# Kernel tuning notes

Measured on AMD Instinct MI355X. Metric: run time of the kernel, lower is better.

## Reference

```python
import jax, jax.numpy as jnp
import numpy as np
from jax import lax

EPS = 1e-5

def conv3x3(x, w, b):
    # x: [N,C,H,W], w: [O,I,3,3]
    y = lax.conv_general_dilated(x, w, window_strides=(1, 1), padding='SAME',
                                 dimension_numbers=('NCHW', 'OIHW', 'NCHW'))
    return y + b[None, :, None, None]

def batchnorm(x, gamma, beta):
    # training-mode BN: batch statistics over (N,H,W), biased variance
    mean = x.mean(axis=(0, 2, 3), keepdims=True)
    var = x.var(axis=(0, 2, 3), keepdims=True)
    xn = (x - mean) * lax.rsqrt(var + EPS)
    return xn * gamma[None, :, None, None] + beta[None, :, None, None]

def instance_norm_unbiased(x):
    # per-(sample, channel) mean and unbiased std (torch .std() default ddof=1)
    n = x.shape[2] * x.shape[3]
    m = x.mean(axis=(2, 3), keepdims=True)
    var = ((x - m) ** 2).sum(axis=(2, 3), keepdims=True) / (n - 1)
    return (x - m) / jnp.sqrt(var)

def res_block(x, w, b, g, be):
    # w: [2,64,64,3,3]; b,g,be: [2,64]
    h = x
    for k in range(2):
        h = jax.nn.celu(batchnorm(conv3x3(h, w[k], b[k]), g[k], be[k]))
    return h + x

def setup_inputs() -> dict:
    key = jax.random.key(0)
    ks = jax.random.split(key, 8)
    x = jax.random.normal(ks[0], (8, 3, 256, 256), dtype=jnp.float32)
    w1 = jax.random.normal(ks[1], (64, 6, 3, 3), dtype=jnp.float32) * 0.05
    b1 = jnp.zeros((64,), jnp.float32)
    g1 = jnp.ones((64,), jnp.float32)
    be1 = jnp.zeros((64,), jnp.float32)
    bw = jax.random.normal(ks[2], (3, 2, 64, 64, 3, 3), dtype=jnp.float32) * 0.02
    bb = jnp.zeros((3, 2, 64), jnp.float32)
    bg = jnp.ones((3, 2, 64), jnp.float32)
    bbe = jnp.zeros((3, 2, 64), jnp.float32)
    w2 = jax.random.normal(ks[3], (3, 64, 3, 3), dtype=jnp.float32) * 0.05
    b2 = jnp.zeros((3,), jnp.float32)
    return {"x": x, "w1": w1, "b1": b1, "g1": g1, "be1": be1,
            "bw": bw, "bb": bb, "bg": bg, "bbe": bbe, "w2": w2, "b2": b2}

def reference(x, w1, b1, g1, be1, bw, bb, bg, bbe, w2, b2):
    normalized = instance_norm_unbiased(x)
    inp = jnp.concatenate([x, normalized], axis=1)  # [N,6,H,W]
    out = jax.nn.celu(batchnorm(conv3x3(inp, w1, b1), g1, be1))
    for i in range(3):  # 3 structurally distinct ResBlocks
        out = res_block(out, bw[i], bb[i], bg[i], bbe[i])
    out = jax.nn.celu(conv3x3(out, w2, b2))
    return out + x
```

## Files before the change

kernel.cpp:

```cpp
#include <hip/hip_runtime.h>
#include <cstdint>
#include <cstddef>

#define DEVI __device__ __forceinline__

static constexpr int HW = 65536;
static constexpr float PTOTF = 524288.0f;
static constexpr int NPB = 8192;

typedef __attribute__((ext_vector_type(8))) short bfx8;
typedef __attribute__((ext_vector_type(16))) float fx16;
typedef __attribute__((ext_vector_type(4))) float fx4;

DEVI unsigned short f2bf(float f) {
  unsigned int x = __float_as_uint(f);
  x += 0x7fffu + ((x >> 16) & 1u);
  return (unsigned short)(x >> 16);
}
DEVI float celuf(float v) { return v > 0.0f ? v : expm1f(v); }

DEVI void unpack8(const uint4 u, float* v) {
  v[0] = __uint_as_float(u.x << 16); v[1] = __uint_as_float(u.x & 0xffff0000u);
  v[2] = __uint_as_float(u.y << 16); v[3] = __uint_as_float(u.y & 0xffff0000u);
  v[4] = __uint_as_float(u.z << 16); v[5] = __uint_as_float(u.z & 0xffff0000u);
  v[6] = __uint_as_float(u.w << 16); v[7] = __uint_as_float(u.w & 0xffff0000u);
}

DEVI void gload16(const unsigned short* g, unsigned short* l) {
  __builtin_amdgcn_global_load_lds(
      (const __attribute__((address_space(1))) unsigned int*)g,
      (__attribute__((address_space(3))) unsigned int*)l, 16, 0, 0);
}

DEVI size_t padpx(int n, int h, int w) {
  return ((size_t)n * 258 + (h + 1)) * 258 + (w + 1);
}

__global__ __launch_bounds__(256)
void k_prep(const float* __restrict__ w1, const float* __restrict__ bw,
            const float* __restrict__ w2, unsigned short* __restrict__ wc1,
            unsigned short* __restrict__ wtm, unsigned short* __restrict__ wlast,
            unsigned short* a, unsigned short* b, unsigned short* c) {
  int id = blockIdx.x * 256 + threadIdx.x;
  if (id < 24672) {
    const int buf = id / 8224, r = id - buf * 8224;
    const int n = r / 1028, k = r - n * 1028;
    int hp, wp;
    if (k < 258)      { hp = 0;           wp = k; }
    else if (k < 516) { hp = 257;         wp = k - 258; }
    else if (k < 772) { hp = k - 516 + 1; wp = 0; }
    else              { hp = k - 772 + 1; wp = 257; }
    unsigned short* p = (buf == 0 ? a : buf == 1 ? b : c) +
                        (((size_t)n * 258 + hp) * 258 + wp) * 64;
    const uint4 z = {0, 0, 0, 0};
#pragma unroll
    for (int q = 0; q < 8; ++q) ((uint4*)p)[q] = z;
    return;
  }
  id -= 24672;
  if (id < 221184) {
    const int cv = id / 36864, r = id - cv * 36864;
    const int tap = r >> 12, rr = r & 4095, oc = rr >> 6, ic = rr & 63;
    const float v = bw[((size_t)cv * 4096 + oc * 64 + ic) * 9 + tap];
    const int dic = ((((ic >> 3) ^ (oc & 7)) << 3) | (ic & 7));
    wtm[(size_t)cv * 36864 + tap * 4096 + oc * 64 + dic] = f2bf(v);
    return;
  }
  id -= 221184;
  if (id < 5120) {
    const int cch = id >> 10, rr = id & 1023;
    const int m = rr >> 9, l = (rr >> 3) & 63, j = rr & 7;
    const int oc = m * 32 + (l & 31);
    const int tap = 2 * cch + (l >> 5);
    wc1[id] = (tap < 9 && j < 6) ? f2bf(w1[(oc * 6 + j) * 9 + tap])
                                 : (unsigned short)0;
    return;
  }
  id -= 5120;
  if (id < 9216) {
    const int cch = id >> 9, r = id & 511, l = r >> 3, j = r & 7;
    const int oc = l & 15, kg = l >> 4;
    const int tap = cch >> 1, kc = cch & 1;
    const int ic = kc * 32 + kg * 8 + j;
    wlast[id] = (oc < 3) ? f2bf(w2[(oc * 64 + ic) * 9 + tap]) : (unsigned short)0;
  }
}

__global__ __launch_bounds__(256)
void k_inorm(const float* __restrict__ x, float* __restrict__ ms) {
  __shared__ float s1[256], s2[256];
  const int b = blockIdx.x;
  const float4* p = (const float4*)(x + (size_t)b * HW);
  float sum = 0.f, sq = 0.f;
  for (int j = threadIdx.x; j < HW / 4; j += 256) {
    const float4 v = p[j];
    sum += v.x + v.y + v.z + v.w;
    sq  += v.x * v.x + v.y * v.y + v.z * v.z + v.w * v.w;
  }
  s1[threadIdx.x] = sum; s2[threadIdx.x] = sq;
  __syncthreads();
  for (int s = 128; s > 0; s >>= 1) {
    if ((int)threadIdx.x < s) {
      s1[threadIdx.x] += s1[threadIdx.x + s];
      s2[threadIdx.x] += s2[threadIdx.x + s];
    }
    __syncthreads();
  }
  if (threadIdx.x == 0) {
    const float m = s1[0] * (1.0f / HW);
    const float var = (s2[0] - s1[0] * s1[0] * (1.0f / HW)) * (1.0f / (HW - 1));
    ms[2 * b] = m;
    ms[2 * b + 1] = rsqrtf(var);
  }
}

__global__ __launch_bounds__(256)
void k_conv1(const float* __restrict__ x, const float* __restrict__ ms,
             const unsigned short* __restrict__ wc1, unsigned short* __restrict__ out,
             float* __restrict__ psum, float* __restrict__ psq) {
  __shared__ __align__(16) unsigned short in_s[6 * 66 * 8];
  __shared__ float s_red[2][4][64];

  const int t = threadIdx.x;
  const int lane = t & 63, wv = t >> 6;
  const int l31 = lane & 31, hi = lane >> 5;
  const int b = blockIdx.x;
  const int n = b >> 8;
  const int h0 = ((b >> 2) & 63) * 4;
  const int w0 = (b & 3) * 64;

  const float m0 = ms[6 * n + 0], r0 = ms[6 * n + 1];
  const float m1 = ms[6 * n + 2], r1 = ms[6 * n + 3];
  const float m2 = ms[6 * n + 4], r2 = ms[6 * n + 5];

  for (int id = t; id < 396; id += 256) {
    const int r = id / 66, px = id - r * 66;
    const int gh = h0 + r - 1, gw = w0 + px - 1;
    uint4 u = {0, 0, 0, 0};
    if (((unsigned)gh < 256u) && ((unsigned)gw < 256u)) {
      const float* xp = x + (size_t)n * 3 * HW + gh * 256 + gw;
      const float a0 = xp[0], a1 = xp[HW], a2 = xp[2 * HW];
      const float n0 = (a0 - m0) * r0, n1 = (a1 - m1) * r1, n2 = (a2 - m2) * r2;
      u.x = (unsigned)f2bf(a0) | ((unsigned)f2bf(a1) << 16);
      u.y = (unsigned)f2bf(a2) | ((unsigned)f2bf(n0) << 16);
      u.z = (unsigned)f2bf(n1) | ((unsigned)f2bf(n2) << 16);
    }
    *(uint4*)(in_s + (size_t)id * 8) = u;
  }
  __syncthreads();

  fx16 acc[2][2] = {};
#pragma unroll
  for (int c = 0; c < 5; ++c) {
    bfx8 af[2];
#pragma unroll
    for (int m = 0; m < 2; ++m)
      af[m] = *(const bfx8*)(wc1 + ((size_t)(c * 2 + m) * 64 + lane) * 8);
    const int tap = 2 * c + hi;
    const int dh = (tap < 9) ? tap / 3 : 0;
    const int dw = (tap < 9) ? (tap - (tap / 3) * 3) : 0;
    bfx8 bf[2];
#pragma unroll
    for (int p = 0; p < 2; ++p) {
      const int px = p * 32 + l31 + dw;
      bf[p] = *(const bfx8*)(in_s + ((size_t)(wv + dh) * 66 + px) * 8);
    }
#pragma unroll
    for (int m = 0; m < 2; ++m)
#pragma unroll
      for (int p = 0; p < 2; ++p)
        acc[m][p] = __builtin_amdgcn_mfma_f32_32x32x16_bf16(
            af[m], bf[p], acc[m][p], 0, 0, 0);
  }

  const size_t obase = (((size_t)n * 258 + (h0 + wv + 1)) * 258 + (w0 + 1)) * 64;
  float sv[2][16], qv[2][16];
#pragma unroll
  for (int m = 0; m < 2; ++m) {
#pragma unroll
    for (int p = 0; p < 2; ++p) {
      const int px = p * 32 + l31;
#pragma unroll
      for (int q = 0; q < 4; ++q) {
        const int ocb = m * 32 + q * 8 + 4 * hi;
        ushort4 o;
        o.x = f2bf(acc[m][p][q * 4 + 0]);
        o.y = f2bf(acc[m][p][q * 4 + 1]);
        o.z = f2bf(acc[m][p][q * 4 + 2]);
        o.w = f2bf(acc[m][p][q * 4 + 3]);
        *(ushort4*)(out + obase + (size_t)px * 64 + ocb) = o;
      }
    }
#pragma unroll
    for (int r = 0; r < 16; ++r) {
      const float a0 = acc[m][0][r], a1 = acc[m][1][r];
      sv[m][r] = a0 + a1;
      qv[m][r] = a0 * a0 + a1 * a1;
    }
  }
#pragma unroll
  for (int st = 1; st <= 16; st <<= 1)
#pragma unroll
    for (int m = 0; m < 2; ++m)
#pragma unroll
      for (int r = 0; r < 16; ++r) {
        sv[m][r] += __shfl_xor(sv[m][r], st);
        qv[m][r] += __shfl_xor(qv[m][r], st);
      }
  if (l31 == 0) {
#pragma unroll
    for (int m = 0; m < 2; ++m)
#pragma unroll
      for (int r = 0; r < 16; ++r) {
        const int oc = m * 32 + (r & 3) + 8 * (r >> 2) + 4 * hi;
        s_red[0][wv][oc] = sv[m][r];
        s_red[1][wv][oc] = qv[m][r];
      }
  }
  __syncthreads();
  if (t < 64) {
    psum[(size_t)t * NPB + b] = s_red[0][0][t] + s_red[0][1][t] +
                                s_red[0][2][t] + s_red[0][3][t];
    psq [(size_t)t * NPB + b] = s_red[1][0][t] + s_red[1][1][t] +
                                s_red[1][2][t] + s_red[1][3][t];
  }
}

__global__ __launch_bounds__(512, 2)
void k_mconv(const unsigned short* __restrict__ in,
             const unsigned short* __restrict__ wt,
             unsigned short* __restrict__ out,
             float* __restrict__ psum, float* __restrict__ psq) {
  __shared__ __align__(16) unsigned short w_s[36864];
  __shared__ __align__(16) unsigned short ring[10 * 528 * 8];
  __shared__ float s_red[2][8][64];

  const int t = threadIdx.x;
  const int lane = t & 63, wv = t >> 6;
  const int l31 = lane & 31, hi = lane >> 5;
  const int row = wv >> 1;
  const int m   = wv & 1;
  const int bo = blockIdx.x;
  const int b = (bo & 7) * 64 + (bo >> 3);
  const int n  = b >> 6;
  const int hb = (b >> 2) & 15;
  const int w0 = (b & 3) * 64;
  const int oc = m * 32 + l31;

#pragma unroll
  for (int j = 0; j < 9; ++j) {
    const int id = t + j * 512;
    gload16(wt + (size_t)id * 8, w_s + (size_t)id * 8);
  }
  {
    const size_t gb = ((size_t)n * 258 + hb * 16) * 258 + w0;
#pragma unroll
    for (int j = 0; j < 7; ++j) {
      const int id = t + j * 512;
      if (id < 3168) {
        const int r = id / 528, c = id - r * 528;
        const int px = c >> 3;
        const int R = r * 66 + px;
        const int sl = (c & 7) ^ (R & 7);
        gload16(in + (gb + (size_t)r * 258 + px) * 64 + sl * 8,
                ring + (size_t)id * 8);
      }
    }
  }

  float sv[16] = {0.f}, qv[16] = {0.f};

  for (int k = 0; k < 4; ++k) {
    if (k == 0) { asm volatile("s_waitcnt vmcnt(0)" ::: "memory"); }
    else       { asm volatile("s_waitcnt vmcnt(8)" ::: "memory"); }
    __builtin_amdgcn_sched_barrier(0);
    __builtin_amdgcn_s_barrier();
    __builtin_amdgcn_sched_barrier(0);
    if (k < 3) {
      const int base = 4 * k + 6;
#pragma unroll
      for (int j = 0; j < 5; ++j) {
        const int id = t + j * 512;
        if (id < 2112) {
          const int r = id / 528, c = id - r * 528;
          const int Lr = base + r;
          const int s = (Lr >= 10) ? Lr - 10 : Lr;
          const int px = c >> 3;
          const int R = s * 66 + px;
          const int sl = (c & 7) ^ (R & 7);
          gload16(in + (((size_t)n * 258 + hb * 16 + Lr) * 258 + w0 + px) * 64 + sl * 8,
                  ring + ((size_t)s * 528 + c) * 8);
        }
      }
    }
    __builtin_amdgcn_sched_barrier(0);

    fx16 acc[2] = {};
#pragma unroll
    for (int tap = 0; tap < 9; ++tap) {
      const int dh = tap / 3, dw = tap - dh * 3;
      const int Lr = 4 * k + row + dh;
      const int s = (Lr >= 10) ? Lr - 10 : Lr;
      const int Rbase = s * 66 + dw;
#pragma unroll
      for (int ks = 0; ks < 4; ++ks) {
        const int slW = (ks * 2 + hi) ^ (oc & 7);
        const bfx8 wf = *(const bfx8*)((const char*)w_s +
                         ((size_t)tap * 4096 + oc * 64) * 2 + (slW << 4));
        bfx8 bf[2];
#pragma unroll
        for (int p = 0; p < 2; ++p) {
          const int R = Rbase + p * 32 + l31;
          const int slA = (ks * 2 + hi) ^ (R & 7);
          bf[p] = *(const bfx8*)((const char*)ring + (size_t)R * 128 + (slA << 4));
        }
#pragma unroll
        for (int p = 0; p < 2; ++p)
          acc[p] = __builtin_amdgcn_mfma_f32_32x32x16_bf16(
              wf, bf[p], acc[p], 0, 0, 0);
      }
    }

    const int orow = hb * 16 + 4 * k + row + 1;
    const size_t obase = (((size_t)n * 258 + orow) * 258 + (w0 + 1)) * 64;
#pragma unroll
    for (int p = 0; p < 2; ++p) {
      const int px = p * 32 + l31;
#pragma unroll
      for (int q = 0; q < 4; ++q) {
        const int ocb = m * 32 + q * 8 + 4 * hi;
        ushort4 o;
        o.x = f2bf(acc[p][q * 4 + 0]);
        o.y = f2bf(acc[p][q * 4 + 1]);
        o.z = f2bf(acc[p][q * 4 + 2]);
        o.w = f2bf(acc[p][q * 4 + 3]);
        *(ushort4*)(out + obase + (size_t)px * 64 + ocb) = o;
      }
    }
#pragma unroll
    for (int r = 0; r < 16; ++r) {
      const float a0 = acc[0][r], a1 = acc[1][r];
      sv[r] += a0 + a1;
      qv[r] += a0 * a0 + a1 * a1;
    }
  }

#pragma unroll
  for (int st = 1; st <= 16; st <<= 1)
#pragma unroll
    for (int r = 0; r < 16; ++r) {
      sv[r] += __shfl_xor(sv[r], st);
      qv[r] += __shfl_xor(qv[r], st);
    }
  if (l31 == 0) {
#pragma unroll
    for (int r = 0; r < 16; ++r) {
      const int oc2 = m * 32 + (r & 3) + 8 * (r >> 2) + 4 * hi;
      s_red[0][wv][oc2] = sv[r];
      s_red[1][wv][oc2] = qv[r];
    }
  }
  __syncthreads();
  if (t < 64) {
    const int mm = t >> 5;
    psum[(size_t)t * NPB + bo] = s_red[0][0 * 2 + mm][t] + s_red[0][1 * 2 + mm][t] +
                                 s_red[0][2 * 2 + mm][t] + s_red[0][3 * 2 + mm][t];
    psq [(size_t)t * NPB + bo] = s_red[1][0 * 2 + mm][t] + s_red[1][1 * 2 + mm][t] +
                                 s_red[1][2 * 2 + mm][t] + s_red[1][3 * 2 + mm][t];
  }
}

__global__ __launch_bounds__(256)
void k_bnfin(const float* __restrict__ psum, const float* __restrict__ psq,
             const float* __restrict__ g, const float* __restrict__ be,
             float* __restrict__ bnp, int nb) {
  __shared__ float s1[256], s2[256];
  const int c = blockIdx.x;
  const int t = threadIdx.x;
  float s = 0.f, q = 0.f;
  for (int j = t; j < nb; j += 256) {
    s += psum[(size_t)c * NPB + j];
    q += psq[(size_t)c * NPB + j];
  }
  s1[t] = s; s2[t] = q;
  __syncthreads();
  for (int st = 128; st > 0; st >>= 1) {
    if (t < st) { s1[t] += s1[t + st]; s2[t] += s2[t + st]; }
    __syncthreads();
  }
  if (t == 0) {
    const float m = s1[0] / PTOTF;
    const float var = s2[0] / PTOTF - m * m;
    const float sc = g[c] * rsqrtf(var + 1e-5f);
    bnp[c] = sc;
    bnp[64 + c] = be[c] - m * sc;
  }
}

template<int RES>
__global__ __launch_bounds__(256)
void k_apply(const unsigned short* __restrict__ y, const float* __restrict__ bnp,
             unsigned short* __restrict__ a) {
  const size_t gid = (size_t)blockIdx.x * 256 + threadIdx.x;
  const int px = (int)(gid >> 3);
  const int c0 = ((int)gid & 7) * 8;
  const int n = px >> 16, hh = (px >> 8) & 255, ww = px & 255;
  const size_t i = padpx(n, hh, ww) * 64 + c0;
  float v[8];
  unpack8(*(const uint4*)(y + i), v);
  const float4 sa = *(const float4*)(bnp + c0);
  const float4 sb = *(const float4*)(bnp + c0 + 4);
  const float4 ha = *(const float4*)(bnp + 64 + c0);
  const float4 hb = *(const float4*)(bnp + 64 + c0 + 4);
  const float sc[8] = {sa.x, sa.y, sa.z, sa.w, sb.x, sb.y, sb.z, sb.w};
  const float sh[8] = {ha.x, ha.y, ha.z, ha.w, hb.x, hb.y, hb.z, hb.w};
  float r[8];
#pragma unroll
  for (int q = 0; q < 8; ++q) r[q] = celuf(v[q] * sc[q] + sh[q]);
  if (RES) {
    float av[8];
    unpack8(*(const uint4*)(a + i), av);
#pragma unroll
    for (int q = 0; q < 8; ++q) r[q] += av[q];
  }
  uint4 o;
  o.x = (unsigned)f2bf(r[0]) | ((unsigned)f2bf(r[1]) << 16);
  o.y = (unsigned)f2bf(r[2]) | ((unsigned)f2bf(r[3]) << 16);
  o.z = (unsigned)f2bf(r[4]) | ((unsigned)f2bf(r[5]) << 16);
  o.w = (unsigned)f2bf(r[6]) | ((unsigned)f2bf(r[7]) << 16);
  *(uint4*)(a + i) = o;
}

__global__ __launch_bounds__(256, 2)
void k_last(const unsigned short* __restrict__ a, const float* __restrict__ x,
            const unsigned short* __restrict__ wl, const float* __restrict__ b2,
            float* __restrict__ outp) {
  __shared__ __align__(16) unsigned short a_s[3168 * 8];

  const int t = threadIdx.x;
  const int lane = t & 63, wv = t >> 6;
  int b = blockIdx.x;
  b = (b & 7) * 256 + (b >> 3);
  const int n  = b >> 8;
  const int h0 = ((b >> 2) & 63) * 4;
  const int w0 = (b & 3) * 64;

  const size_t ibase = ((size_t)n * 258 + h0) * 258 + w0;
  for (int seg = wv; seg < 54; seg += 4) {
    const int r = seg / 9;
    const int p = seg - r * 9;
    const int c = p * 64 + lane;
    const int px = c >> 3;
    const int R = r * 66 + px;
    const int sl = (c & 7) ^ (R & 7);
    if (c < 528)
      gload16(a + (ibase + (size_t)r * 258 + px) * 64 + sl * 8,
              a_s + (size_t)(r * 528 + p * 64) * 8);
  }
  __syncthreads();

  const int col = lane & 15, kg = lane >> 4;
  const float bz0 = b2[0], bz1 = b2[1], bz2 = b2[2];
#pragma unroll
  for (int ti = 0; ti < 4; ++ti) {
    fx4 acc = {};
#pragma unroll
    for (int tap = 0; tap < 9; ++tap) {
      const int dh = tap / 3, dw = tap - dh * 3;
      const int px = ti * 16 + col + dw;
      const int R = (wv + dh) * 66 + px;
#pragma unroll
      for (int kc = 0; kc < 2; ++kc) {
        const int s = kc * 4 + kg;
        const bfx8 bf = *(const bfx8*)((const char*)a_s +
            (size_t)R * 128 + ((s ^ (R & 7)) << 4));
        const bfx8 af = *(const bfx8*)(wl + ((size_t)(tap * 2 + kc) * 64 + lane) * 8);
        acc = __builtin_amdgcn_mfma_f32_16x16x32_bf16(af, bf, acc, 0, 0, 0);
      }
    }
    if (kg == 0) {
      const int h = h0 + wv;
      const size_t ob = (size_t)n * 3 * HW + ((size_t)h << 8) + w0 + ti * 16 + col;
      outp[ob]          = celuf(acc[0] + bz0) + x[ob];
      outp[ob + HW]     = celuf(acc[1] + bz1) + x[ob + HW];
      outp[ob + 2 * HW] = celuf(acc[2] + bz2) + x[ob + 2 * HW];
    }
  }
}

extern "C" void kernel_launch(void* const* d_in, const int* in_sizes, int n_in,
                              void* d_out, int out_size, void* d_ws, size_t ws_size,
                              hipStream_t stream) {
  const float* x   = (const float*)d_in[0];
  const float* w1  = (const float*)d_in[1];
  const float* g1  = (const float*)d_in[3];
  const float* be1 = (const float*)d_in[4];
  const float* bw  = (const float*)d_in[5];
  const float* bg  = (const float*)d_in[7];
  const float* bbe = (const float*)d_in[8];
  const float* w2  = (const float*)d_in[9];
  const float* b2  = (const float*)d_in[10];
  float* out = (float*)d_out;

  const size_t PADBUF = (size_t)8 * 258 * 258 * 64 * 2;
  size_t off = 0;
  auto alloc = [&](size_t bytes) {
    size_t cur = off;
    off += (bytes + 255) & ~(size_t)255;
    return cur;
  };
  const size_t oA   = alloc(PADBUF);
  const size_t oB   = alloc(PADBUF);
  const size_t oC   = alloc(PADBUF);
  const size_t oW1  = alloc(5120 * 2);
  const size_t oWM  = alloc((size_t)6 * 36864 * 2);
  const size_t oWL  = alloc(9216 * 2);
  const size_t oMS  = alloc(48 * 4);
  const size_t oBNP = alloc(7 * 128 * 4);
  const size_t oPS  = alloc((size_t)64 * NPB * 4);
  const size_t oPQ  = alloc((size_t)64 * NPB * 4);
  if (off > ws_size) return;

  char* wsb = (char*)d_ws;
  unsigned short* bufA = (unsigned short*)(wsb + oA);
  unsigned short* bufB = (unsigned short*)(wsb + oB);
  unsigned short* bufC = (unsigned short*)(wsb + oC);
  unsigned short* wc1 = (unsigned short*)(wsb + oW1);
  unsigned short* wtm = (unsigned short*)(wsb + oWM);
  unsigned short* wlast = (unsigned short*)(wsb + oWL);
  float* ms  = (float*)(wsb + oMS);
  float* bnp = (float*)(wsb + oBNP);
  float* psum = (float*)(wsb + oPS);
  float* psq  = (float*)(wsb + oPQ);

  k_prep<<<1017, 256, 0, stream>>>(w1, bw, w2, wc1, wtm, wlast, bufA, bufB, bufC);
  k_inorm<<<24, 256, 0, stream>>>(x, ms);

  k_conv1<<<2048, 256, 0, stream>>>(x, ms, wc1, bufB, psum, psq);
  k_bnfin<<<64, 256, 0, stream>>>(psum, psq, g1, be1, bnp, 2048);
  k_apply<0><<<16384, 256, 0, stream>>>(bufB, bnp, bufA);

  for (int i = 0; i < 3; ++i) {
    const int s1 = 1 + 2 * i, s2 = 2 + 2 * i;
    k_mconv<<<512, 512, 0, stream>>>(bufA, wtm + (size_t)(2 * i) * 36864,
                                     bufB, psum, psq);
    k_bnfin<<<64, 256, 0, stream>>>(psum, psq, bg + (size_t)(2 * i) * 64,
        bbe + (size_t)(2 * i) * 64, bnp + (size_t)s1 * 128, 512);
    k_apply<0><<<16384, 256, 0, stream>>>(bufB, bnp + (size_t)s1 * 128, bufC);
    k_mconv<<<512, 512, 0, stream>>>(bufC, wtm + (size_t)(2 * i + 1) * 36864,
                                     bufB, psum, psq);
    k_bnfin<<<64, 256, 0, stream>>>(psum, psq, bg + (size_t)(2 * i + 1) * 64,
        bbe + (size_t)(2 * i + 1) * 64, bnp + (size_t)s2 * 128, 512);
    k_apply<1><<<16384, 256, 0, stream>>>(bufB, bnp + (size_t)s2 * 128, bufA);
  }

  k_last<<<2048, 256, 0, stream>>>(bufA, x, wlast, b2, out);
}
```

Before: 676.6 us.

## Fuse BN+CELU apply into second resblock conv's input staging

The second convolution of each residual block now reads the raw pre-BN conv output and applies batchnorm scale/shift plus CELU while staging tiles into LDS. Halo pixels are forced to zero. This removes one full-tensor apply kernel (a read and a write of the activation) per resblock. The price is that the fused conv switches from async global-to-LDS loads to register-staged loads with ALU work interleaved between MFMA phases, which may reduce load/compute overlap.

```diff
diff --git a/kernel.cpp b/kernel.cpp
--- a/kernel.cpp
+++ b/kernel.cpp
@@ -24,6 +24,14 @@
   v[2] = __uint_as_float(u.y << 16); v[3] = __uint_as_float(u.y & 0xffff0000u);
   v[4] = __uint_as_float(u.z << 16); v[5] = __uint_as_float(u.z & 0xffff0000u);
   v[6] = __uint_as_float(u.w << 16); v[7] = __uint_as_float(u.w & 0xffff0000u);
+}
+DEVI uint4 pack8(const float* v) {
+  uint4 o;
+  o.x = (unsigned)f2bf(v[0]) | ((unsigned)f2bf(v[1]) << 16);
+  o.y = (unsigned)f2bf(v[2]) | ((unsigned)f2bf(v[3]) << 16);
+  o.z = (unsigned)f2bf(v[4]) | ((unsigned)f2bf(v[5]) << 16);
+  o.w = (unsigned)f2bf(v[6]) | ((unsigned)f2bf(v[7]) << 16);
+  return o;
 }
 
 DEVI void gload16(const unsigned short* g, unsigned short* l) {
@@ -226,14 +234,16 @@
   }
 }
 
+template<int MODE>
 __global__ __launch_bounds__(512, 2)
-void k_mconv(const unsigned short* __restrict__ in,
+void k_mconv(const unsigned short* __restrict__ in, const float* __restrict__ bnp,
              const unsigned short* __restrict__ wt,
              unsigned short* __restrict__ out,
              float* __restrict__ psum, float* __restrict__ psq) {
   __shared__ __align__(16) unsigned short w_s[36864];
   __shared__ __align__(16) unsigned short ring[10 * 528 * 8];
   __shared__ float s_red[2][8][64];
+  __shared__ float s_bnp[128];
 
   const int t = threadIdx.x;
   const int lane = t & 63, wv = t >> 6;
@@ -252,7 +262,8 @@
     const int id = t + j * 512;
     gload16(wt + (size_t)id * 8, w_s + (size_t)id * 8);
   }
-  {
+
+  if constexpr (MODE == 1) {
     const size_t gb = ((size_t)n * 258 + hb * 16) * 258 + w0;
 #pragma unroll
     for (int j = 0; j < 7; ++j) {
@@ -266,34 +277,83 @@
                 ring + (size_t)id * 8);
       }
     }
+  } else {
+    if (t < 128) s_bnp[t] = bnp[t];
+    __syncthreads();
+    const size_t gb = ((size_t)n * 258 + hb * 16) * 258 + w0;
+    for (int id = t; id < 3168; id += 512) {
+      const int r = id / 528, c = id - r * 528;
+      const int px = c >> 3;
+      const int R = r * 66 + px;
+      const int sl = (c & 7) ^ (R & 7);
+      const int hp = hb * 16 + r, wp = w0 + px;
+      const bool pad = (hp == 0) | (hp == 257) | (wp == 0) | (wp == 257);
+      const uint4 u = *(const uint4*)(in + (gb + (size_t)r * 258 + px) * 64 + sl * 8);
+      float v[8];
+      unpack8(u, v);
+      const int ch0 = sl * 8;
+#pragma unroll
+      for (int q = 0; q < 8; ++q) {
+        const float z = v[q] * s_bnp[ch0 + q] + s_bnp[64 + ch0 + q];
+        v[q] = pad ? 0.f : celuf(z);
+      }
+      *(uint4*)(ring + ((size_t)r * 528 + c) * 8) = pack8(v);
+    }
   }
 
   float sv[16] = {0.f}, qv[16] = {0.f};
 
   for (int k = 0; k < 4; ++k) {
-    if (k == 0) { asm volatile("s_waitcnt vmcnt(0)" ::: "memory"); }
-    else       { asm volatile("s_waitcnt vmcnt(8)" ::: "memory"); }
-    __builtin_amdgcn_sched_barrier(0);
-    __builtin_amdgcn_s_barrier();
-    __builtin_amdgcn_sched_barrier(0);
-    if (k < 3) {
-      const int base = 4 * k + 6;
-#pragma unroll
-      for (int j = 0; j < 5; ++j) {
-        const int id = t + j * 512;
-        if (id < 2112) {
-          const int r = id / 528, c = id - r * 528;
-          const int Lr = base + r;
-          const int s = (Lr >= 10) ? Lr - 10 : Lr;
-          const int px = c >> 3;
-          const int R = s * 66 + px;
-          const int sl = (c & 7) ^ (R & 7);
-          gload16(in + (((size_t)n * 258 + hb * 16 + Lr) * 258 + w0 + px) * 64 + sl * 8,
-                  ring + ((size_t)s * 528 + c) * 8);
+    if constexpr (MODE == 1) {
+      if (k == 0) { asm volatile("s_waitcnt vmcnt(0)" ::: "memory"); }
+      else       { asm volatile("s_waitcnt vmcnt(8)" ::: "memory"); }
+      __builtin_amdgcn_sched_barrier(0);
+      __builtin_amdgcn_s_barrier();
+      __builtin_amdgcn_sched_barrier(0);
+      if (k < 3) {
+        const int base = 4 * k + 6;
+#pragma unroll
+        for (int j = 0; j < 5; ++j) {
+          const int id = t + j * 512;
+          if (id < 2112) {
+            const int r = id / 528, c = id - r * 528;
+            const int Lr = base + r;
+            const int s = (Lr >= 10) ? Lr - 10 : Lr;
+            const int px = c >> 3;
+            const int R = s * 66 + px;
+            const int sl = (c & 7) ^ (R & 7);
+            gload16(in + (((size_t)n * 258 + hb * 16 + Lr) * 258 + w0 + px) * 64 + sl * 8,
+                    ring + ((size_t)s * 528 + c) * 8);
+          }
         }
       }
-    }
-    __builtin_amdgcn_sched_barrier(0);
+      __builtin_amdgcn_sched_barrier(0);
+    } else {
+      if (k == 0) {
+        __syncthreads();
+      }
+    }
+
+    uint4 stg[5];
+    if constexpr (MODE == 2) {
+      if (k < 3) {
+        const int base = 4 * k + 6;
+#pragma unroll
+        for (int j = 0; j < 5; ++j) {
+          const int id = t + j * 512;
+          if (id < 2112) {
+            const int r = id / 528, c = id - r * 528;
+            const int Lr = base + r;
+            const int s = (Lr >= 10) ? Lr - 10 : Lr;
+            const int px = c >> 3;
+            const int R = s * 66 + px;
+            const int sl = (c & 7) ^ (R & 7);
+            stg[j] = *(const uint4*)(in +
+                (((size_t)n * 258 + hb * 16 + Lr) * 258 + w0 + px) * 64 + sl * 8);
+          }
+        }
+      }
+    }
 
     fx16 acc[2] = {};
 #pragma unroll
@@ -342,6 +402,39 @@
       const float a0 = acc[0][r], a1 = acc[1][r];
       sv[r] += a0 + a1;
       qv[r] += a0 * a0 + a1 * a1;
+    }
+
+    if constexpr (MODE == 2) {
+      if (k < 3) {
+        const int base = 4 * k + 6;
+#pragma unroll
+        for (int j = 0; j < 5; ++j) {
+          const int id = t + j * 512;
+          if (id < 2112) {
+            const int r = id / 528, c = id - r * 528;
+            const int Lr = base + r;
+            const int s = (Lr >= 10) ? Lr - 10 : Lr;
+            const int px = c >> 3;
+            const int R = s * 66 + px;
+            const int sl = (c & 7) ^ (R & 7);
+            const int hp = hb * 16 + Lr, wp = w0 + px;
+            const bool pad = (hp == 0) | (hp == 257) | (wp == 0) | (wp == 257);
+            float v[8];
+            unpack8(stg[j], v);
+            const int ch0 = sl * 8;
+#pragma unroll
+            for (int q = 0; q < 8; ++q) {
+              const float z = v[q] * s_bnp[ch0 + q] + s_bnp[64 + ch0 + q];
+              v[q] = pad ? 0.f : celuf(z);
+            }
+            *(uint4*)(ring + ((size_t)s * 528 + c) * 8) = pack8(v);
+          }
+        }
+        asm volatile("s_waitcnt lgkmcnt(0)" ::: "memory");
+      }
+      __builtin_amdgcn_sched_barrier(0);
+      __builtin_amdgcn_s_barrier();
+      __builtin_amdgcn_sched_barrier(0);
     }
   }
 
@@ -423,12 +516,7 @@
 #pragma unroll
     for (int q = 0; q < 8; ++q) r[q] += av[q];
   }
-  uint4 o;
-  o.x = (unsigned)f2bf(r[0]) | ((unsigned)f2bf(r[1]) << 16);
-  o.y = (unsigned)f2bf(r[2]) | ((unsigned)f2bf(r[3]) << 16);
-  o.z = (unsigned)f2bf(r[4]) | ((unsigned)f2bf(r[5]) << 16);
-  o.w = (unsigned)f2bf(r[6]) | ((unsigned)f2bf(r[7]) << 16);
-  *(uint4*)(a + i) = o;
+  *(uint4*)(a + i) = pack8(r);
 }
 
 __global__ __launch_bounds__(256, 2)
@@ -542,16 +630,15 @@
 
   for (int i = 0; i < 3; ++i) {
     const int s1 = 1 + 2 * i, s2 = 2 + 2 * i;
-    k_mconv<<<512, 512, 0, stream>>>(bufA, wtm + (size_t)(2 * i) * 36864,
-                                     bufB, psum, psq);
+    k_mconv<1><<<512, 512, 0, stream>>>(bufA, nullptr,
+        wtm + (size_t)(2 * i) * 36864, bufB, psum, psq);
     k_bnfin<<<64, 256, 0, stream>>>(psum, psq, bg + (size_t)(2 * i) * 64,
         bbe + (size_t)(2 * i) * 64, bnp + (size_t)s1 * 128, 512);
-    k_apply<0><<<16384, 256, 0, stream>>>(bufB, bnp + (size_t)s1 * 128, bufC);
-    k_mconv<<<512, 512, 0, stream>>>(bufC, wtm + (size_t)(2 * i + 1) * 36864,
-                                     bufB, psum, psq);
+    k_mconv<2><<<512, 512, 0, stream>>>(bufB, bnp + (size_t)s1 * 128,
+        wtm + (size_t)(2 * i + 1) * 36864, bufC, psum, psq);
     k_bnfin<<<64, 256, 0, stream>>>(psum, psq, bg + (size_t)(2 * i + 1) * 64,
         bbe + (size_t)(2 * i + 1) * 64, bnp + (size_t)s2 * 128, 512);
-    k_apply<1><<<16384, 256, 0, stream>>>(bufB, bnp + (size_t)s2 * 128, bufA);
+    k_apply<1><<<16384, 256, 0, stream>>>(bufC, bnp + (size_t)s2 * 128, bufA);
   }
 
   k_last<<<2048, 256, 0, stream>>>(bufA, x, wlast, b2, out);
```

Result: slower. 788.6 us (+16.6%).
